# Kernel optimization log

Measured on AMD Instinct MI355X. Metric: run time of the kernel, lower is better.

The kernel has to match this reference:

```python
import jax, jax.numpy as jnp
import numpy as np

N = 50000      # num nodes
E = 800000     # num edges
DIN = 64       # in_channels
H = 128        # hidden_channels
L = 3          # num GCN layers


def setup_inputs() -> dict:
    key = jax.random.key(0)
    ks = jax.random.split(key, 18)
    x = jax.random.normal(ks[0], (N, DIN), jnp.float32)
    edge_index = jax.random.randint(ks[1], (2, E), 0, N, dtype=jnp.int32)
    s_in = 1.0 / np.sqrt(DIN)
    s_h = 1.0 / np.sqrt(H)
    W_in = jax.random.normal(ks[2], (DIN, H), jnp.float32) * s_in
    b_in = jnp.zeros((H,), jnp.float32)
    Wc = jax.random.normal(ks[3], (L, H, H), jnp.float32) * s_h
    bc = jnp.zeros((L, H), jnp.float32)
    gamma = 1.0 + 0.1 * jax.random.normal(ks[4], (L, H), jnp.float32)
    beta = 0.1 * jax.random.normal(ks[5], (L, H), jnp.float32)
    rmean = 0.1 * jax.random.normal(ks[6], (L, H), jnp.float32)
    rvar = jax.random.uniform(ks[7], (L, H), jnp.float32, 0.5, 1.5)
    W1 = jax.random.normal(ks[8], (H, H // 2), jnp.float32) * s_h
    b1 = jnp.zeros((H // 2,), jnp.float32)
    W2 = jax.random.normal(ks[9], (H // 2, 1), jnp.float32) * (1.0 / np.sqrt(H // 2))
    b2 = jnp.zeros((1,), jnp.float32)
    return dict(x=x, edge_index=edge_index, W_in=W_in, b_in=b_in, Wc=Wc, bc=bc,
                gamma=gamma, beta=beta, rmean=rmean, rvar=rvar,
                W1=W1, b1=b1, W2=W2, b2=b2)


def reference(x, edge_index, W_in, b_in, Wc, bc, gamma, beta, rmean, rvar, W1, b1, W2, b2):
    n = x.shape[0]
    loops = jnp.arange(n, dtype=edge_index.dtype)
    src = jnp.concatenate([edge_index[0], loops])  # [E+N]
    dst = jnp.concatenate([edge_index[1], loops])
    # symmetric GCN normalization with self-loops
    deg = jax.ops.segment_sum(jnp.ones(src.shape[0], jnp.float32), dst, num_segments=n)
    dis = jnp.where(deg > 0, jax.lax.rsqrt(jnp.maximum(deg, 1.0)), 0.0)
    norm = (dis[src] * dis[dst])[:, None]  # [E+N, 1]
    eps = 1e-5

    h = jax.nn.relu(x @ W_in + b_in)  # [N, H]
    for i in range(Wc.shape[0]):
        h_in = h
        hw = h @ Wc[i]                                   # [N, H]
        agg = jax.ops.segment_sum(hw[src] * norm, dst, num_segments=n) + bc[i]
        hbn = (agg - rmean[i]) * jax.lax.rsqrt(rvar[i] + eps) * gamma[i] + beta[i]
        h = jax.nn.relu(hbn)
        if i > 0:
            h = h + h_in  # residual (skipped on first layer, as in source)
        # dropout: eval mode -> identity
    out = jax.nn.relu(h @ W1 + b1) @ W2 + b2  # [N, 1]
    return out.squeeze(-1)
```

## Files before the change

kernel.cpp:

```cpp
#include <hip/hip_runtime.h>


__device__ __forceinline__ void fma4(float4& acc, float s, const float4& v) {
    acc.x = fmaf(s, v.x, acc.x);
    acc.y = fmaf(s, v.y, acc.y);
    acc.z = fmaf(s, v.z, acc.z);
    acc.w = fmaf(s, v.w, acc.w);
}
__device__ __forceinline__ void add4(float4& acc, const float4& v) {
    acc.x += v.x; acc.y += v.y; acc.z += v.z; acc.w += v.w;
}

constexpr int DIN_C = 64;
constexpr int H_C = 128;


__global__ __launch_bounds__(256) void count_deg_kernel(const int* __restrict__ dst,
                                                        int* __restrict__ cnt, int e) {
    int i = blockIdx.x * 256 + threadIdx.x;
    if (i < e) atomicAdd(&cnt[dst[i]], 1);
}

__global__ __launch_bounds__(512) void scan_blocks_kernel(const int* __restrict__ cnt,
                                                          int* __restrict__ excl,
                                                          int* __restrict__ bsums, int n) {
    __shared__ int s[2][512];
    int t = threadIdx.x;
    int i = blockIdx.x * 512 + t;
    int v = (i < n) ? cnt[i] : 0;
    s[0][t] = v;
    __syncthreads();
    int cur = 0;
    for (int off = 1; off < 512; off <<= 1) {
        int x = s[cur][t];
        if (t >= off) x += s[cur][t - off];
        s[cur ^ 1][t] = x;
        cur ^= 1;
        __syncthreads();
    }
    if (i < n) excl[i] = s[cur][t] - v;
    if (t == 511) bsums[blockIdx.x] = s[cur][t];
}

__global__ __launch_bounds__(128) void scan_tops_kernel(const int* __restrict__ bsums,
                                                        int* __restrict__ btops, int nb) {
    __shared__ int s[2][128];
    int t = threadIdx.x;
    int v = (t < nb) ? bsums[t] : 0;
    s[0][t] = v;
    __syncthreads();
    int cur = 0;
    for (int off = 1; off < 128; off <<= 1) {
        int x = s[cur][t];
        if (t >= off) x += s[cur][t - off];
        s[cur ^ 1][t] = x;
        cur ^= 1;
        __syncthreads();
    }
    if (t < nb) btops[t] = s[cur][t] - v;
}

__global__ __launch_bounds__(512) void finalize_nodes_kernel(
        const int* __restrict__ excl, const int* __restrict__ btops,
        const int* __restrict__ cnt, int* __restrict__ row_ptr,
        int* __restrict__ cursor, float* __restrict__ dis, int n, int e) {
    int i = blockIdx.x * 512 + threadIdx.x;
    if (i < n) {
        int rp = excl[i] + btops[blockIdx.x];
        row_ptr[i] = rp;
        cursor[i]  = rp;
        dis[i] = rsqrtf((float)(cnt[i] + 1));
    }
    if (i == 0) row_ptr[n] = e;
}

__global__ __launch_bounds__(256) void fill_csr_kernel(
        const int* __restrict__ src, const int* __restrict__ dst,
        int* __restrict__ cursor, int* __restrict__ csr_src, int e) {
    int i = blockIdx.x * 256 + threadIdx.x;
    if (i < e) {
        int s = src[i], d = dst[i];
        int pos = atomicAdd(&cursor[d], 1);
        csr_src[pos] = s;
    }
}


template <int K, int NC, bool RELU, bool BIAS, bool SCALE>
__global__ __launch_bounds__(256) void gemm_kernel(
        const float* __restrict__ A, const float* __restrict__ W,
        const float* __restrict__ bias, const float* __restrict__ rs,
        float* __restrict__ C, int M) {
    constexpr int CG  = NC / 4;
    constexpr int RG  = 256 / CG;
    constexpr int RPB = RG * 8;
    const int t  = threadIdx.x;
    const int tx = t % CG;
    const int ty = t / CG;
    const int c  = tx * 4;
    const int r0 = blockIdx.x * RPB + ty * 8;

    float4 bv = {0.f, 0.f, 0.f, 0.f};
    if (BIAS) bv = *(const float4*)&bias[c];

    if (r0 + 8 <= M) {
        float4 acc[8];
#pragma unroll
        for (int i = 0; i < 8; ++i) acc[i] = bv;
        const float* Ar = A + (size_t)r0 * K;
#pragma unroll 2
        for (int k0 = 0; k0 < K; k0 += 4) {
            float4 w0 = *(const float4*)&W[(size_t)(k0 + 0) * NC + c];
            float4 w1 = *(const float4*)&W[(size_t)(k0 + 1) * NC + c];
            float4 w2 = *(const float4*)&W[(size_t)(k0 + 2) * NC + c];
            float4 w3 = *(const float4*)&W[(size_t)(k0 + 3) * NC + c];
#pragma unroll
            for (int i = 0; i < 8; ++i) {
                float4 a = *(const float4*)&Ar[(size_t)i * K + k0];
                fma4(acc[i], a.x, w0);
                fma4(acc[i], a.y, w1);
                fma4(acc[i], a.z, w2);
                fma4(acc[i], a.w, w3);
            }
        }
        float* Cr = C + (size_t)r0 * NC + c;
#pragma unroll
        for (int i = 0; i < 8; ++i) {
            float4 v = acc[i];
            if (RELU) {
                v.x = fmaxf(v.x, 0.f); v.y = fmaxf(v.y, 0.f);
                v.z = fmaxf(v.z, 0.f); v.w = fmaxf(v.w, 0.f);
            }
            if (SCALE) {
                float s = rs[r0 + i];
                v.x *= s; v.y *= s; v.z *= s; v.w *= s;
            }
            *(float4*)&Cr[(size_t)i * NC] = v;
        }
    } else {
        for (int i = 0; i < 8; ++i) {
            int r = r0 + i;
            if (r >= M) break;
            float4 acc = bv;
            const float* Ar = A + (size_t)r * K;
            for (int k0 = 0; k0 < K; k0 += 4) {
                float4 a  = *(const float4*)&Ar[k0];
                float4 w0 = *(const float4*)&W[(size_t)(k0 + 0) * NC + c];
                float4 w1 = *(const float4*)&W[(size_t)(k0 + 1) * NC + c];
                float4 w2 = *(const float4*)&W[(size_t)(k0 + 2) * NC + c];
                float4 w3 = *(const float4*)&W[(size_t)(k0 + 3) * NC + c];
                fma4(acc, a.x, w0);
                fma4(acc, a.y, w1);
                fma4(acc, a.z, w2);
                fma4(acc, a.w, w3);
            }
            if (RELU) {
                acc.x = fmaxf(acc.x, 0.f); acc.y = fmaxf(acc.y, 0.f);
                acc.z = fmaxf(acc.z, 0.f); acc.w = fmaxf(acc.w, 0.f);
            }
            if (SCALE) {
                float s = rs[r];
                acc.x *= s; acc.y *= s; acc.z *= s; acc.w *= s;
            }
            *(float4*)&C[(size_t)r * NC + c] = acc;
        }
    }
}


__global__ __launch_bounds__(256) void agg_bn_kernel(
        const float* __restrict__ hwp, const int* __restrict__ row_ptr,
        const int* __restrict__ csr_src, const float* __restrict__ dis,
        const float* __restrict__ bc, const float* __restrict__ gamma_,
        const float* __restrict__ beta_, const float* __restrict__ rmean,
        const float* __restrict__ rvar,
        const float* __restrict__ h_in, float* __restrict__ h_out,
        int n, int residual) {
    int wid  = (blockIdx.x * 256 + threadIdx.x) >> 6;
    int lane = threadIdx.x & 63;
    if (wid >= n) return;
    const int half = lane >> 5;
    const int f    = (lane & 31) * 4;

    float4 a0 = {0.f, 0.f, 0.f, 0.f};
    float4 a1 = {0.f, 0.f, 0.f, 0.f};
    if (half == 0) a0 = *(const float4*)(hwp + (size_t)wid * H_C + f);

    const int beg = row_ptr[wid], end = row_ptr[wid + 1];
    int e = beg + half;
    for (; e + 2 < end; e += 4) {
        int s0 = csr_src[e];
        int s1 = csr_src[e + 2];
        float4 r0 = *(const float4*)(hwp + (size_t)s0 * H_C + f);
        float4 r1 = *(const float4*)(hwp + (size_t)s1 * H_C + f);
        add4(a0, r0);
        add4(a1, r1);
    }
    if (e < end) {
        int s = csr_src[e];
        float4 r = *(const float4*)(hwp + (size_t)s * H_C + f);
        add4(a0, r);
    }
    add4(a0, a1);
    a0.x += __shfl_xor(a0.x, 32);
    a0.y += __shfl_xor(a0.y, 32);
    a0.z += __shfl_xor(a0.z, 32);
    a0.w += __shfl_xor(a0.w, 32);

    if (half == 0) {
        const float eps = 1e-5f;
        float dd = dis[wid];
        float4 b4 = *(const float4*)&bc[f];
        float4 g4 = *(const float4*)&gamma_[f];
        float4 be4 = *(const float4*)&beta_[f];
        float4 m4 = *(const float4*)&rmean[f];
        float4 v4 = *(const float4*)&rvar[f];
        float4 o;
        o.x = fmaf((fmaf(dd, a0.x, b4.x) - m4.x) * rsqrtf(v4.x + eps), g4.x, be4.x);
        o.y = fmaf((fmaf(dd, a0.y, b4.y) - m4.y) * rsqrtf(v4.y + eps), g4.y, be4.y);
        o.z = fmaf((fmaf(dd, a0.z, b4.z) - m4.z) * rsqrtf(v4.z + eps), g4.z, be4.z);
        o.w = fmaf((fmaf(dd, a0.w, b4.w) - m4.w) * rsqrtf(v4.w + eps), g4.w, be4.w);
        o.x = fmaxf(o.x, 0.f); o.y = fmaxf(o.y, 0.f);
        o.z = fmaxf(o.z, 0.f); o.w = fmaxf(o.w, 0.f);
        if (residual) {
            float4 r = *(const float4*)(h_in + (size_t)wid * H_C + f);
            add4(o, r);
        }
        *(float4*)(h_out + (size_t)wid * H_C + f) = o;
    }
}


__global__ __launch_bounds__(256) void final_dot_kernel(
        const float* __restrict__ t, const float* __restrict__ W2,
        const float* __restrict__ b2, float* __restrict__ out, int n) {
    int wid  = (blockIdx.x * 256 + threadIdx.x) >> 6;
    int lane = threadIdx.x & 63;
    if (wid >= n) return;
    float v = t[(size_t)wid * 64 + lane] * W2[lane];
#pragma unroll
    for (int off = 32; off > 0; off >>= 1) v += __shfl_down(v, off, 64);
    if (lane == 0) out[wid] = v + b2[0];
}


extern "C" void kernel_launch(void* const* d_in, const int* in_sizes, int n_in,
                              void* d_out, int out_size, void* d_ws, size_t ws_size,
                              hipStream_t stream) {
    const float* x      = (const float*)d_in[0];
    const int*   ei     = (const int*)  d_in[1];
    const float* W_in   = (const float*)d_in[2];
    const float* b_in   = (const float*)d_in[3];
    const float* Wc     = (const float*)d_in[4];
    const float* bc     = (const float*)d_in[5];
    const float* gamma_ = (const float*)d_in[6];
    const float* beta_  = (const float*)d_in[7];
    const float* rmean  = (const float*)d_in[8];
    const float* rvar   = (const float*)d_in[9];
    const float* W1     = (const float*)d_in[10];
    const float* b1     = (const float*)d_in[11];
    const float* W2     = (const float*)d_in[12];
    const float* b2     = (const float*)d_in[13];
    float* out = (float*)d_out;

    const int M = in_sizes[0] / DIN_C;
    const int E = in_sizes[1] / 2;
    const int* src = ei;
    const int* dst = ei + E;

    size_t off = 0;
    auto alloc = [&](size_t bytes) {
        void* p = (char*)d_ws + off;
        off += (bytes + 255) & ~(size_t)255;
        return p;
    };
    int*   cnt      = (int*)  alloc((size_t)M * 4);
    int*   excl     = (int*)  alloc((size_t)M * 4);
    int*   bsums    = (int*)  alloc(512);
    int*   btops    = (int*)  alloc(512);
    int*   row_ptr  = (int*)  alloc((size_t)(M + 1) * 4);
    int*   cursor   = (int*)  alloc((size_t)M * 4);
    float* dis      = (float*)alloc((size_t)M * 4);
    int*   csr_src  = (int*)  alloc((size_t)E * 4);
    float* hA       = (float*)alloc((size_t)M * H_C * 4);
    float* hB       = (float*)alloc((size_t)M * H_C * 4);
    float* hw       = (float*)alloc((size_t)M * H_C * 4);
    float* t_buf    = hw;

    const int NB = (M + 511) / 512;

    hipMemsetAsync(cnt, 0, (size_t)M * 4, stream);
    count_deg_kernel<<<(E + 255) / 256, 256, 0, stream>>>(dst, cnt, E);
    scan_blocks_kernel<<<NB, 512, 0, stream>>>(cnt, excl, bsums, M);
    scan_tops_kernel<<<1, 128, 0, stream>>>(bsums, btops, NB);
    finalize_nodes_kernel<<<NB, 512, 0, stream>>>(excl, btops, cnt, row_ptr, cursor, dis, M, E);
    fill_csr_kernel<<<(E + 255) / 256, 256, 0, stream>>>(src, dst, cursor, csr_src, E);

    {
        constexpr int RPB = (256 / (H_C / 4)) * 8;
        gemm_kernel<DIN_C, H_C, true, true, false><<<(M + RPB - 1) / RPB, 256, 0, stream>>>(
            x, W_in, b_in, nullptr, hA, M);
    }

    float* cur = hA;
    float* nxt = hB;
    for (int layer = 0; layer < 3; ++layer) {
        constexpr int RPB = (256 / (H_C / 4)) * 8;
        gemm_kernel<H_C, H_C, false, false, true><<<(M + RPB - 1) / RPB, 256, 0, stream>>>(
            cur, Wc + (size_t)layer * H_C * H_C, nullptr, dis, hw, M);
        agg_bn_kernel<<<(M * 64 + 255) / 256, 256, 0, stream>>>(
            hw, row_ptr, csr_src, dis,
            bc + (size_t)layer * H_C, gamma_ + (size_t)layer * H_C,
            beta_ + (size_t)layer * H_C, rmean + (size_t)layer * H_C,
            rvar + (size_t)layer * H_C,
            cur, nxt, M, layer > 0 ? 1 : 0);
        float* tmp = cur; cur = nxt; nxt = tmp;
    }

    {
        constexpr int RPB = (256 / (64 / 4)) * 8;
        gemm_kernel<H_C, 64, true, true, false><<<(M + RPB - 1) / RPB, 256, 0, stream>>>(
            cur, W1, b1, nullptr, t_buf, M);
    }
    final_dot_kernel<<<(M * 64 + 255) / 256, 256, 0, stream>>>(t_buf, W2, b2, out, M);
}
```

Before: 583.9 us.

## Fuse MLP head into one kernel and deepen gather unroll in aggregation

Replaces the W1 GEMM plus separate final dot kernel with a single head kernel that applies ReLU, dots with W2 in registers and reduces across lanes with shuffles. This removes the write and reread of the intermediate N×64 buffer and one launch. The edge-gather loop in the aggregation kernel is unrolled to four independent accumulators per half-wave to keep more loads in flight, and the GEMM k-loop unroll goes from 2 to 4. The extra unrolling raises register pressure and may reduce occupancy.

```diff
diff --git a/kernel.cpp b/kernel.cpp
--- a/kernel.cpp
+++ b/kernel.cpp
@@ -108,7 +108,7 @@
 #pragma unroll
         for (int i = 0; i < 8; ++i) acc[i] = bv;
         const float* Ar = A + (size_t)r0 * K;
-#pragma unroll 2
+#pragma unroll 4
         for (int k0 = 0; k0 < K; k0 += 4) {
             float4 w0 = *(const float4*)&W[(size_t)(k0 + 0) * NC + c];
             float4 w1 = *(const float4*)&W[(size_t)(k0 + 1) * NC + c];
@@ -168,6 +168,95 @@
 }
 
 
+__global__ __launch_bounds__(256) void head_kernel(
+        const float* __restrict__ A, const float* __restrict__ W1,
+        const float* __restrict__ b1, const float* __restrict__ W2,
+        const float* __restrict__ b2, float* __restrict__ out, int M) {
+    constexpr int K = 128, NC = 64;
+    constexpr int CG  = NC / 4;
+    constexpr int RPB = (256 / CG) * 8;
+    const int t  = threadIdx.x;
+    const int tx = t % CG;
+    const int ty = t / CG;
+    const int c  = tx * 4;
+    const int r0 = blockIdx.x * RPB + ty * 8;
+
+    float4 bv = *(const float4*)&b1[c];
+    float4 w2v = *(const float4*)&W2[c];
+    float b2v = b2[0];
+
+    float part[8];
+    if (r0 + 8 <= M) {
+        float4 acc[8];
+#pragma unroll
+        for (int i = 0; i < 8; ++i) acc[i] = bv;
+        const float* Ar = A + (size_t)r0 * K;
+#pragma unroll 4
+        for (int k0 = 0; k0 < K; k0 += 4) {
+            float4 w0 = *(const float4*)&W1[(size_t)(k0 + 0) * NC + c];
+            float4 w1 = *(const float4*)&W1[(size_t)(k0 + 1) * NC + c];
+            float4 w2 = *(const float4*)&W1[(size_t)(k0 + 2) * NC + c];
+            float4 w3 = *(const float4*)&W1[(size_t)(k0 + 3) * NC + c];
+#pragma unroll
+            for (int i = 0; i < 8; ++i) {
+                float4 a = *(const float4*)&Ar[(size_t)i * K + k0];
+                fma4(acc[i], a.x, w0);
+                fma4(acc[i], a.y, w1);
+                fma4(acc[i], a.z, w2);
+                fma4(acc[i], a.w, w3);
+            }
+        }
+#pragma unroll
+        for (int i = 0; i < 8; ++i) {
+            float4 v = acc[i];
+            v.x = fmaxf(v.x, 0.f); v.y = fmaxf(v.y, 0.f);
+            v.z = fmaxf(v.z, 0.f); v.w = fmaxf(v.w, 0.f);
+            part[i] = v.x * w2v.x + v.y * w2v.y + v.z * w2v.z + v.w * w2v.w;
+        }
+    } else {
+#pragma unroll
+        for (int i = 0; i < 8; ++i) {
+            int r = r0 + i;
+            part[i] = 0.f;
+            if (r < M) {
+                float4 acc = bv;
+                const float* Ar = A + (size_t)r * K;
+                for (int k0 = 0; k0 < K; k0 += 4) {
+                    float4 a  = *(const float4*)&Ar[k0];
+                    float4 w0 = *(const float4*)&W1[(size_t)(k0 + 0) * NC + c];
+                    float4 w1 = *(const float4*)&W1[(size_t)(k0 + 1) * NC + c];
+                    float4 w2 = *(const float4*)&W1[(size_t)(k0 + 2) * NC + c];
+                    float4 w3 = *(const float4*)&W1[(size_t)(k0 + 3) * NC + c];
+                    fma4(acc, a.x, w0);
+                    fma4(acc, a.y, w1);
+                    fma4(acc, a.z, w2);
+                    fma4(acc, a.w, w3);
+                }
+                acc.x = fmaxf(acc.x, 0.f); acc.y = fmaxf(acc.y, 0.f);
+                acc.z = fmaxf(acc.z, 0.f); acc.w = fmaxf(acc.w, 0.f);
+                part[i] = acc.x * w2v.x + acc.y * w2v.y + acc.z * w2v.z + acc.w * w2v.w;
+            }
+        }
+    }
+#pragma unroll
+    for (int i = 0; i < 8; ++i) {
+        float v = part[i];
+        v += __shfl_xor(v, 1);
+        v += __shfl_xor(v, 2);
+        v += __shfl_xor(v, 4);
+        v += __shfl_xor(v, 8);
+        part[i] = v;
+    }
+    if (tx == 0) {
+#pragma unroll
+        for (int i = 0; i < 8; ++i) {
+            int r = r0 + i;
+            if (r < M) out[r] = part[i] + b2v;
+        }
+    }
+}
+
+
 __global__ __launch_bounds__(256) void agg_bn_kernel(
         const float* __restrict__ hwp, const int* __restrict__ row_ptr,
         const int* __restrict__ csr_src, const float* __restrict__ dis,
@@ -184,10 +273,26 @@
 
     float4 a0 = {0.f, 0.f, 0.f, 0.f};
     float4 a1 = {0.f, 0.f, 0.f, 0.f};
+    float4 a2 = {0.f, 0.f, 0.f, 0.f};
+    float4 a3 = {0.f, 0.f, 0.f, 0.f};
     if (half == 0) a0 = *(const float4*)(hwp + (size_t)wid * H_C + f);
 
     const int beg = row_ptr[wid], end = row_ptr[wid + 1];
     int e = beg + half;
+    for (; e + 6 < end; e += 8) {
+        int s0 = csr_src[e];
+        int s1 = csr_src[e + 2];
+        int s2 = csr_src[e + 4];
+        int s3 = csr_src[e + 6];
+        float4 r0 = *(const float4*)(hwp + (size_t)s0 * H_C + f);
+        float4 r1 = *(const float4*)(hwp + (size_t)s1 * H_C + f);
+        float4 r2 = *(const float4*)(hwp + (size_t)s2 * H_C + f);
+        float4 r3 = *(const float4*)(hwp + (size_t)s3 * H_C + f);
+        add4(a0, r0);
+        add4(a1, r1);
+        add4(a2, r2);
+        add4(a3, r3);
+    }
     for (; e + 2 < end; e += 4) {
         int s0 = csr_src[e];
         int s1 = csr_src[e + 2];
@@ -201,6 +306,8 @@
         float4 r = *(const float4*)(hwp + (size_t)s * H_C + f);
         add4(a0, r);
     }
+    add4(a0, a2);
+    add4(a1, a3);
     add4(a0, a1);
     a0.x += __shfl_xor(a0.x, 32);
     a0.y += __shfl_xor(a0.y, 32);
@@ -231,19 +338,6 @@
 }
 
 
-__global__ __launch_bounds__(256) void final_dot_kernel(
-        const float* __restrict__ t, const float* __restrict__ W2,
-        const float* __restrict__ b2, float* __restrict__ out, int n) {
-    int wid  = (blockIdx.x * 256 + threadIdx.x) >> 6;
-    int lane = threadIdx.x & 63;
-    if (wid >= n) return;
-    float v = t[(size_t)wid * 64 + lane] * W2[lane];
-#pragma unroll
-    for (int off = 32; off > 0; off >>= 1) v += __shfl_down(v, off, 64);
-    if (lane == 0) out[wid] = v + b2[0];
-}
-
-
 extern "C" void kernel_launch(void* const* d_in, const int* in_sizes, int n_in,
                               void* d_out, int out_size, void* d_ws, size_t ws_size,
                               hipStream_t stream) {
@@ -285,7 +379,6 @@
     float* hA       = (float*)alloc((size_t)M * H_C * 4);
     float* hB       = (float*)alloc((size_t)M * H_C * 4);
     float* hw       = (float*)alloc((size_t)M * H_C * 4);
-    float* t_buf    = hw;
 
     const int NB = (M + 511) / 512;
 
@@ -319,8 +412,7 @@
 
     {
         constexpr int RPB = (256 / (64 / 4)) * 8;
-        gemm_kernel<H_C, 64, true, true, false><<<(M + RPB - 1) / RPB, 256, 0, stream>>>(
-            cur, W1, b1, nullptr, t_buf, M);
-    }
-    final_dot_kernel<<<(M * 64 + 255) / 256, 256, 0, stream>>>(t_buf, W2, b2, out, M);
-}
+        head_kernel<<<(M + RPB - 1) / RPB, 256, 0, stream>>>(
+            cur, W1, b1, W2, b2, out, M);
+    }
+}
```

Result: faster. 565.7 us (-3.1%).
